# Performance work log

Measured on AMD Instinct MI355X. Metric: run time of the kernel, lower is better.

The kernel has to match this reference:

```python
import jax, jax.numpy as jnp
import numpy as np

N_HEADS = 12
VAL_DIM = 64
TOKEN_DIM = 768


def setup_inputs() -> dict:
    key = jax.random.key(0)
    k1, k2, k3 = jax.random.split(key, 3)
    x = jax.random.normal(k1, (8, 1024, TOKEN_DIM), dtype=jnp.float32)
    W_qkv = jax.random.normal(k2, (TOKEN_DIM, 3 * N_HEADS * VAL_DIM), dtype=jnp.float32) * (TOKEN_DIM ** -0.5)
    W_merge = jax.random.normal(k3, (N_HEADS * VAL_DIM, TOKEN_DIM), dtype=jnp.float32) * ((N_HEADS * VAL_DIM) ** -0.5)
    return {"x": x, "W_qkv": W_qkv, "W_merge": W_merge}


def reference(x, W_qkv, W_merge):
    b, p, _ = x.shape
    scale = VAL_DIM ** -0.5
    qkv = jnp.einsum('bpt,tf->bpf', x, W_qkv)  # (b, p, 3*h*v)
    # einops '(h v k)' -> k is innermost factor
    qkv = qkv.reshape(b, p, N_HEADS, VAL_DIM, 3)
    q = jnp.transpose(qkv[..., 0], (0, 2, 1, 3))  # (b, h, p, v)
    k = jnp.transpose(qkv[..., 1], (0, 2, 1, 3))
    v = jnp.transpose(qkv[..., 2], (0, 2, 1, 3))
    scores = jnp.einsum('bhid,bhjd->bhij', q, k) * scale
    attn = jax.nn.softmax(scores, axis=-1)
    out = jnp.einsum('bhij,bhjd->bhid', attn, v)
    out = jnp.transpose(out, (0, 2, 1, 3)).reshape(b, p, N_HEADS * VAL_DIM)
    return jnp.einsum('bpf,ft->bpt', out, W_merge)
```

## Files before the change

kernel.cpp:

```cpp
#include <hip/hip_runtime.h>
#include <hip/hip_bf16.h>
#include <math.h>


#define B_  8
#define P_  1024
#define T_  768
#define H_  12
#define DV  64
#define F3  2304
#define HD  768
#define PSTR 72

typedef float  f32x4  __attribute__((ext_vector_type(4)));
typedef __bf16 bf16x4 __attribute__((ext_vector_type(4)));
typedef __bf16 bf16x8 __attribute__((ext_vector_type(8)));

#if defined(__has_builtin)
#if __has_builtin(__builtin_amdgcn_exp2f)
#define EX2(x) __builtin_amdgcn_exp2f(x)
#endif
#endif
#ifndef EX2
#define EX2(x) exp2f(x)
#endif

__device__ __forceinline__ void gload16(const void* g, void* l) {
    __builtin_amdgcn_global_load_lds((const __attribute__((address_space(1))) void*)g,
                                     (__attribute__((address_space(3))) void*)l,
                                     16, 0, 0);
}

__global__ __launch_bounds__(256) void k_cvt(const float* __restrict__ src,
                                             __bf16* __restrict__ dst) {
    int bid = blockIdx.x;
    int xcd = bid & 7;
    int seq = bid >> 3;
    int strip = (seq / 12) * 8 + xcd;
    int sub   = seq % 12;
    size_t base = (size_t)strip * (128 * T_) + (size_t)sub * (128 * T_ / 12);
    const float4* s4 = (const float4*)(src + base);
    bf16x4*       d4 = (bf16x4*)(dst + base);
#pragma unroll
    for (int i = 0; i < 8; i++) {
        float4 v = s4[i * 256 + threadIdx.x];
        bf16x4 o = { (__bf16)v.x, (__bf16)v.y, (__bf16)v.z, (__bf16)v.w };
        d4[i * 256 + threadIdx.x] = o;
    }
}

__global__ void k_tcvt(const float* __restrict__ src,
                       __bf16* __restrict__ dst, int R, int C) {
    __shared__ __bf16 tile[32][33];
    int tx = threadIdx.x, ty = threadIdx.y;
    int x = blockIdx.x * 32 + tx;
    int y = blockIdx.y * 32 + ty;
#pragma unroll
    for (int j = 0; j < 32; j += 8)
        tile[ty + j][tx] = (__bf16)src[(size_t)(y + j) * C + x];
    __syncthreads();
    int x2 = blockIdx.y * 32 + tx;
    int y2 = blockIdx.x * 32 + ty;
#pragma unroll
    for (int j = 0; j < 32; j += 8)
        dst[(size_t)(y2 + j) * R + x2] = tile[tx][ty + j];
}

__global__ void k_tcvt_qkv(const float* __restrict__ src,
                           __bf16* __restrict__ dst) {
    __shared__ __bf16 tile[32][33];
    int tx = threadIdx.x, ty = threadIdx.y;
    int n = blockIdx.x * 32 + tx;
    int r = n / 768, idx = n - r * 768;
    int f = (idx >> 6) * 192 + (idx & 63) * 3 + r;
    int t0 = blockIdx.y * 32;
#pragma unroll
    for (int j = 0; j < 32; j += 8)
        tile[ty + j][tx] = (__bf16)src[(size_t)(t0 + ty + j) * F3 + f];
    __syncthreads();
#pragma unroll
    for (int j = 0; j < 32; j += 8)
        dst[(size_t)(blockIdx.x * 32 + ty + j) * T_ + t0 + tx] = tile[tx][ty + j];
}

#define GEMM64_MAINLOOP(Aptr, Btptr, brow, bcol, LD)                             \
    int tid  = threadIdx.x;                                                      \
    int lane = tid & 63, wave = tid >> 6;                                        \
    int l16  = lane & 15, quad = lane >> 4;                                      \
    int wm = (wave >> 1) * 64, wn = (wave & 1) * 64;                             \
    int bro = tid >> 3, bq = tid & 7;                                            \
    f32x4 acc[4][4];                                                             \
    _Pragma("unroll") for (int i = 0; i < 4; i++)                                \
        _Pragma("unroll") for (int j = 0; j < 4; j++)                            \
            acc[i][j] = (f32x4){0.f, 0.f, 0.f, 0.f};                             \
    _Pragma("unroll") for (int it = 0; it < 4; it++) {                           \
        int n = it * 32 + bro;                                                   \
        int gp = bq ^ (n & 7);                                                   \
        gload16((Aptr) + (size_t)((brow) * 128 + n) * (LD) + gp * 8,             \
                LDSb + it * 2048 + tid * 8);                                     \
        gload16((Btptr) + (size_t)((bcol) * 128 + n) * (LD) + gp * 8,            \
                LDSb + 8192 + it * 2048 + tid * 8);                              \
    }                                                                            \
    __syncthreads();                                                             \
    for (int k0 = 0; k0 < (LD); k0 += 64) {                                      \
        int cur = (k0 >> 6) & 1;                                                 \
        __bf16* As = LDSb + cur * 16384;                                         \
        __bf16* Bs = As + 8192;                                                  \
        if (k0 + 64 < (LD)) {                                                    \
            __bf16* Ad = LDSb + (cur ^ 1) * 16384;                               \
            _Pragma("unroll") for (int it = 0; it < 4; it++) {                   \
                int n = it * 32 + bro;                                           \
                int gp = bq ^ (n & 7);                                           \
                gload16((Aptr) + (size_t)((brow) * 128 + n) * (LD) + k0 + 64 + gp * 8, \
                        Ad + it * 2048 + tid * 8);                               \
                gload16((Btptr) + (size_t)((bcol) * 128 + n) * (LD) + k0 + 64 + gp * 8, \
                        Ad + 8192 + it * 2048 + tid * 8);                        \
            }                                                                    \
        }                                                                        \
        _Pragma("unroll") for (int ks = 0; ks < 2; ks++) {                       \
            bf16x8 af[4], bfr[4];                                                \
            _Pragma("unroll") for (int i = 0; i < 4; i++) {                      \
                int r = wm + i * 16 + l16;                                       \
                af[i] = *(const bf16x8*)&As[r * 64 + (((ks * 4 + quad) ^ (r & 7)) << 3)]; \
            }                                                                    \
            _Pragma("unroll") for (int j = 0; j < 4; j++) {                      \
                int r = wn + j * 16 + l16;                                       \
                bfr[j] = *(const bf16x8*)&Bs[r * 64 + (((ks * 4 + quad) ^ (r & 7)) << 3)]; \
            }                                                                    \
            _Pragma("unroll") for (int i = 0; i < 4; i++)                        \
                _Pragma("unroll") for (int j = 0; j < 4; j++)                    \
                    acc[i][j] = __builtin_amdgcn_mfma_f32_16x16x32_bf16(         \
                        af[i], bfr[j], acc[i][j], 0, 0, 0);                      \
        }                                                                        \
        __syncthreads();                                                         \
    }

__global__ __launch_bounds__(256, 2) void k_qkv(const __bf16* __restrict__ Xb,
                                                const __bf16* __restrict__ Wt,
                                                __bf16* __restrict__ Q,
                                                __bf16* __restrict__ K,
                                                __bf16* __restrict__ Vt) {
    __shared__ __align__(16) __bf16 LDSb[2 * 2 * 128 * 64];

    int bid  = blockIdx.x;
    int xcd  = bid & 7;
    int seq  = bid >> 3;
    int brow = (seq / 18) * 8 + xcd;
    int bcol = seq % 18;

    GEMM64_MAINLOOP(Xb, Wt, brow, bcol, T_)

    int region = bcol / 6;
    int b  = brow >> 3;
    int p0 = (brow & 7) * 128;

    if (region < 2) {
        __bf16* D = region == 0 ? Q : K;
        float sc = region == 0 ? 0.1803368801f : 1.0f;
#pragma unroll
        for (int j = 0; j < 4; j++) {
            int idx = (bcol - region * 6) * 128 + wn + j * 16 + l16;
            int h = idx >> 6, v = idx & 63;
            __bf16* Dh = D + ((size_t)(b * H_ + h) * P_) * DV + v;
#pragma unroll
            for (int i = 0; i < 4; i++)
#pragma unroll
                for (int r = 0; r < 4; r++)
                    Dh[(size_t)(p0 + wm + i * 16 + quad * 4 + r) * DV] =
                        (__bf16)(acc[i][j][r] * sc);
        }
    } else {
        __syncthreads();
#pragma unroll
        for (int j = 0; j < 4; j++) {
            int n_loc = wn + j * 16 + l16;
#pragma unroll
            for (int i = 0; i < 4; i++)
#pragma unroll
            for (int r = 0; r < 4; r++) {
                int m_loc = wm + i * 16 + quad * 4 + r;
                int phys  = (m_loc >> 3) ^ (n_loc & 15);
                LDSb[n_loc * 128 + phys * 8 + (m_loc & 7)] = (__bf16)acc[i][j][r];
            }
        }
        __syncthreads();
        int n_loc = tid >> 1, halfm = tid & 1;
        int idx = (bcol - 12) * 128 + n_loc;
        int h = idx >> 6, v = idx & 63;
        __bf16* Dh = Vt + ((size_t)(b * H_ + h) * DV + v) * P_ + p0 + halfm * 64;
#pragma unroll
        for (int i = 0; i < 8; i++) {
            int chunk = halfm * 8 + i;
            int phys  = chunk ^ (n_loc & 15);
            bf16x8 val = *(const bf16x8*)&LDSb[n_loc * 128 + phys * 8];
            *(bf16x8*)(Dh + i * 8) = val;
        }
    }
}

__global__ __launch_bounds__(256, 2) void k_merge(const __bf16* __restrict__ O,
                                                  const __bf16* __restrict__ Wt,
                                                  float* __restrict__ out) {
    __shared__ __align__(16) __bf16 LDSb[2 * 2 * 128 * 64];

    int bid  = blockIdx.x;
    int xcd  = bid & 7;
    int seq  = bid >> 3;
    int brow = (seq / 6) * 8 + xcd;
    int bcol = seq % 6;

    GEMM64_MAINLOOP(O, Wt, brow, bcol, HD)

#pragma unroll
    for (int i = 0; i < 4; i++)
#pragma unroll
        for (int j = 0; j < 4; j++) {
            int col = bcol * 128 + wn + j * 16 + l16;
#pragma unroll
            for (int r = 0; r < 4; r++) {
                size_t row = (size_t)(brow * 128 + wm + i * 16 + quad * 4 + r);
                out[row * HD + col] = acc[i][j][r];
            }
        }
}

__global__ __launch_bounds__(256, 6) void k_attn(const __bf16* __restrict__ Q,
                                                 const __bf16* __restrict__ Kb,
                                                 const __bf16* __restrict__ Vt,
                                                 __bf16* __restrict__ O) {
    __shared__ __align__(16) __bf16 Ks[64 * 64];
    __shared__ __align__(16) __bf16 Vs[64 * 64];
    __shared__ __align__(16) __bf16 Pb[4][16 * PSTR];

    int tid  = threadIdx.x;
    int lane = tid & 63, wave = tid >> 6;
    int l16  = lane & 15, quad = lane >> 4;

    int bid = blockIdx.x;
    int xcd = bid & 7;
    int seq = bid >> 3;
    int bh  = xcd * 12 + (seq % 12);
    int qt  = seq / 12;
    int b   = bh / H_, h = bh % H_;

    const __bf16* Qb  = Q  + (size_t)bh * P_ * DV;
    const __bf16* Kbh = Kb + (size_t)bh * P_ * DV;
    const __bf16* Vbh = Vt + (size_t)bh * DV * P_;
    int m0 = qt * 64 + wave * 16;

    bf16x8 a0 = *(const bf16x8*)(Qb + (size_t)(m0 + l16) * DV + quad * 8);
    bf16x8 a1 = *(const bf16x8*)(Qb + (size_t)(m0 + l16) * DV + 32 + quad * 8);

    int l8 = lane >> 3, q8 = lane & 7;

    bf16x8 ones;
#pragma unroll
    for (int i = 0; i < 8; i++) ones[i] = (__bf16)1.0f;

    __bf16* Pw = &Pb[wave][0];
    f32x4 facc = {0.f, 0.f, 0.f, 0.f};
    f32x4 oacc[4] = {{0.f,0.f,0.f,0.f},{0.f,0.f,0.f,0.f},{0.f,0.f,0.f,0.f},{0.f,0.f,0.f,0.f}};
    int swq = l16 & 7;

    for (int c = 0; c < P_; c += 64) {
        __syncthreads();
#pragma unroll
        for (int i = 0; i < 2; i++) {
            int t = wave * 2 + i;
            int r = t * 8 + l8;
            int j = q8 ^ (r & 7);
            gload16(Kbh + (size_t)(c + r) * DV + j * 8, Ks + t * 512 + lane * 8);
            gload16(Vbh + (size_t)r * P_ + c + j * 8,  Vs + t * 512 + lane * 8);
        }
        __syncthreads();

        f32x4 s[4];
#pragma unroll
        for (int ct = 0; ct < 4; ct++) {
            int R = ct * 16 + l16;
            bf16x8 b0 = *(const bf16x8*)&Ks[R * 64 + ((quad ^ swq) * 8)];
            bf16x8 b1 = *(const bf16x8*)&Ks[R * 64 + (((4 + quad) ^ swq) * 8)];
            f32x4 z = {0.f, 0.f, 0.f, 0.f};
            z = __builtin_amdgcn_mfma_f32_16x16x32_bf16(b0, a0, z, 0, 0, 0);
            s[ct] = __builtin_amdgcn_mfma_f32_16x16x32_bf16(b1, a1, z, 0, 0, 0);
        }

#pragma unroll
        for (int ct = 0; ct < 4; ct++) {
            bf16x4 pk;
#pragma unroll
            for (int r = 0; r < 4; r++)
                pk[r] = (__bf16)EX2(s[ct][r]);
            *(bf16x4*)&Pw[l16 * PSTR + ct * 16 + quad * 4] = pk;
        }

#pragma unroll
        for (int ks = 0; ks < 2; ks++) {
            bf16x8 pfrag = *(const bf16x8*)&Pw[l16 * PSTR + ks * 32 + quad * 8];
            facc = __builtin_amdgcn_mfma_f32_16x16x32_bf16(ones, pfrag, facc, 0, 0, 0);
#pragma unroll
            for (int nt = 0; nt < 4; nt++) {
                int R = nt * 16 + l16;
                bf16x8 av = *(const bf16x8*)&Vs[R * 64 + (((ks * 4 + quad) ^ swq) * 8)];
                oacc[nt] = __builtin_amdgcn_mfma_f32_16x16x32_bf16(av, pfrag, oacc[nt], 0, 0, 0);
            }
        }
    }

    float inv = 1.0f / facc[0];

    int p = m0 + l16;
    __bf16* Orow = O + ((size_t)b * P_ + p) * HD + h * DV;
#pragma unroll
    for (int nt = 0; nt < 4; nt++) {
        bf16x4 o4;
#pragma unroll
        for (int r = 0; r < 4; r++) o4[r] = (__bf16)(oacc[nt][r] * inv);
        *(bf16x4*)&Orow[nt * 16 + quad * 4] = o4;
    }
}

extern "C" void kernel_launch(void* const* d_in, const int* in_sizes, int n_in,
                              void* d_out, int out_size, void* d_ws, size_t ws_size,
                              hipStream_t stream) {
    const float* x      = (const float*)d_in[0];
    const float* wqkv   = (const float*)d_in[1];
    const float* wmerge = (const float*)d_in[2];

    char* w = (char*)d_ws;
    __bf16* Xb  = (__bf16*)w;  w += (size_t)B_ * P_ * T_ * 2;
    __bf16* WqT = (__bf16*)w;  w += (size_t)F3 * T_ * 2;
    __bf16* WmT = (__bf16*)w;  w += (size_t)HD * T_ * 2;
    __bf16* Q   = (__bf16*)w;  w += (size_t)B_ * H_ * P_ * DV * 2;
    __bf16* K   = (__bf16*)w;  w += (size_t)B_ * H_ * P_ * DV * 2;
    __bf16* Vt  = (__bf16*)w;  w += (size_t)B_ * H_ * P_ * DV * 2;
    __bf16* O   = (__bf16*)w;

    hipLaunchKernelGGL(k_cvt, dim3(768), dim3(256), 0, stream, x, Xb);

    dim3 tb(32, 8);
    hipLaunchKernelGGL(k_tcvt_qkv, dim3(F3 / 32, T_ / 32), tb, 0, stream, wqkv, WqT);
    hipLaunchKernelGGL(k_tcvt,     dim3(HD / 32, T_ / 32), tb, 0, stream, wmerge, WmT, T_, HD);

    hipLaunchKernelGGL(k_qkv, dim3((B_ * P_ / 128) * (F3 / 128)), dim3(256), 0, stream,
                       Xb, WqT, Q, K, Vt);

    hipLaunchKernelGGL(k_attn, dim3(B_ * H_ * (P_ / 64)), dim3(256), 0, stream,
                       Q, K, Vt, O);

    hipLaunchKernelGGL(k_merge, dim3((B_ * P_ / 128) * (HD / 128)), dim3(256), 0, stream,
                       O, WmT, (float*)d_out);
}
```

Measured before the change: 183.0 us.

## Double query rows per wave and double-buffer K/V tiles in attention

Each wave in the attention kernel now processes 32 query rows instead of 16, so every K/V tile staged in shared memory feeds twice as many MFMAs, and the grid is halved. K/V tiles are double-buffered: the next 64-key chunk is prefetched into the alternate buffer while the current one is computed, leaving one barrier per iteration instead of two. In exchange, register and LDS use per block rise, occupancy bounds drop from 6 to 3 blocks, and there are fewer blocks to spread across CUs.

```diff
diff --git a/kernel.cpp b/kernel.cpp
--- a/kernel.cpp
+++ b/kernel.cpp
@@ -224,13 +224,12 @@
         }
 }
 
-__global__ __launch_bounds__(256, 6) void k_attn(const __bf16* __restrict__ Q,
+__global__ __launch_bounds__(256, 3) void k_attn(const __bf16* __restrict__ Q,
                                                  const __bf16* __restrict__ Kb,
                                                  const __bf16* __restrict__ Vt,
                                                  __bf16* __restrict__ O) {
-    __shared__ __align__(16) __bf16 Ks[64 * 64];
-    __shared__ __align__(16) __bf16 Vs[64 * 64];
-    __shared__ __align__(16) __bf16 Pb[4][16 * PSTR];
+    __shared__ __align__(16) __bf16 KV[2][8192];
+    __shared__ __align__(16) __bf16 Pb[4][2][16 * PSTR];
 
     int tid  = threadIdx.x;
     int lane = tid & 63, wave = tid >> 6;
@@ -246,10 +245,12 @@
     const __bf16* Qb  = Q  + (size_t)bh * P_ * DV;
     const __bf16* Kbh = Kb + (size_t)bh * P_ * DV;
     const __bf16* Vbh = Vt + (size_t)bh * DV * P_;
-    int m0 = qt * 64 + wave * 16;
-
-    bf16x8 a0 = *(const bf16x8*)(Qb + (size_t)(m0 + l16) * DV + quad * 8);
-    bf16x8 a1 = *(const bf16x8*)(Qb + (size_t)(m0 + l16) * DV + 32 + quad * 8);
+    int m0 = qt * 128 + wave * 32;
+
+    bf16x8 a00 = *(const bf16x8*)(Qb + (size_t)(m0 + l16) * DV + quad * 8);
+    bf16x8 a01 = *(const bf16x8*)(Qb + (size_t)(m0 + l16) * DV + 32 + quad * 8);
+    bf16x8 a10 = *(const bf16x8*)(Qb + (size_t)(m0 + 16 + l16) * DV + quad * 8);
+    bf16x8 a11 = *(const bf16x8*)(Qb + (size_t)(m0 + 16 + l16) * DV + 32 + quad * 8);
 
     int l8 = lane >> 3, q8 = lane & 7;
 
@@ -257,66 +258,110 @@
 #pragma unroll
     for (int i = 0; i < 8; i++) ones[i] = (__bf16)1.0f;
 
-    __bf16* Pw = &Pb[wave][0];
-    f32x4 facc = {0.f, 0.f, 0.f, 0.f};
-    f32x4 oacc[4] = {{0.f,0.f,0.f,0.f},{0.f,0.f,0.f,0.f},{0.f,0.f,0.f,0.f},{0.f,0.f,0.f,0.f}};
+    __bf16* Pw0 = &Pb[wave][0][0];
+    __bf16* Pw1 = &Pb[wave][1][0];
+    f32x4 facc0 = {0.f,0.f,0.f,0.f}, facc1 = {0.f,0.f,0.f,0.f};
+    f32x4 oacc0[4] = {{0.f,0.f,0.f,0.f},{0.f,0.f,0.f,0.f},{0.f,0.f,0.f,0.f},{0.f,0.f,0.f,0.f}};
+    f32x4 oacc1[4] = {{0.f,0.f,0.f,0.f},{0.f,0.f,0.f,0.f},{0.f,0.f,0.f,0.f},{0.f,0.f,0.f,0.f}};
     int swq = l16 & 7;
 
-    for (int c = 0; c < P_; c += 64) {
-        __syncthreads();
-#pragma unroll
-        for (int i = 0; i < 2; i++) {
-            int t = wave * 2 + i;
-            int r = t * 8 + l8;
-            int j = q8 ^ (r & 7);
-            gload16(Kbh + (size_t)(c + r) * DV + j * 8, Ks + t * 512 + lane * 8);
-            gload16(Vbh + (size_t)r * P_ + c + j * 8,  Vs + t * 512 + lane * 8);
-        }
-        __syncthreads();
-
-        f32x4 s[4];
+#pragma unroll
+    for (int i = 0; i < 2; i++) {
+        int t8 = wave * 2 + i;
+        int r  = t8 * 8 + l8;
+        int j  = q8 ^ (r & 7);
+        gload16(Kbh + (size_t)r * DV + j * 8, &KV[0][t8 * 512 + lane * 8]);
+        gload16(Vbh + (size_t)r * P_ + j * 8, &KV[0][4096 + t8 * 512 + lane * 8]);
+    }
+    __syncthreads();
+
+    for (int t = 0; t < 16; t++) {
+        int cur = t & 1;
+        const __bf16* Ks = &KV[cur][0];
+        const __bf16* Vs = &KV[cur][4096];
+
+        if (t < 15) {
+            __bf16* Kd = &KV[cur ^ 1][0];
+            int c = (t + 1) * 64;
+#pragma unroll
+            for (int i = 0; i < 2; i++) {
+                int t8 = wave * 2 + i;
+                int r  = t8 * 8 + l8;
+                int j  = q8 ^ (r & 7);
+                gload16(Kbh + (size_t)(c + r) * DV + j * 8, Kd + t8 * 512 + lane * 8);
+                gload16(Vbh + (size_t)r * P_ + c + j * 8,  Kd + 4096 + t8 * 512 + lane * 8);
+            }
+        }
+
+        f32x4 s0[4], s1[4];
 #pragma unroll
         for (int ct = 0; ct < 4; ct++) {
             int R = ct * 16 + l16;
             bf16x8 b0 = *(const bf16x8*)&Ks[R * 64 + ((quad ^ swq) * 8)];
             bf16x8 b1 = *(const bf16x8*)&Ks[R * 64 + (((4 + quad) ^ swq) * 8)];
-            f32x4 z = {0.f, 0.f, 0.f, 0.f};
-            z = __builtin_amdgcn_mfma_f32_16x16x32_bf16(b0, a0, z, 0, 0, 0);
-            s[ct] = __builtin_amdgcn_mfma_f32_16x16x32_bf16(b1, a1, z, 0, 0, 0);
+            f32x4 z0 = {0.f, 0.f, 0.f, 0.f};
+            z0 = __builtin_amdgcn_mfma_f32_16x16x32_bf16(b0, a00, z0, 0, 0, 0);
+            z0 = __builtin_amdgcn_mfma_f32_16x16x32_bf16(b1, a01, z0, 0, 0, 0);
+            s0[ct] = z0;
+            f32x4 z1 = {0.f, 0.f, 0.f, 0.f};
+            z1 = __builtin_amdgcn_mfma_f32_16x16x32_bf16(b0, a10, z1, 0, 0, 0);
+            z1 = __builtin_amdgcn_mfma_f32_16x16x32_bf16(b1, a11, z1, 0, 0, 0);
+            s1[ct] = z1;
         }
 
 #pragma unroll
         for (int ct = 0; ct < 4; ct++) {
-            bf16x4 pk;
-#pragma unroll
-            for (int r = 0; r < 4; r++)
-                pk[r] = (__bf16)EX2(s[ct][r]);
-            *(bf16x4*)&Pw[l16 * PSTR + ct * 16 + quad * 4] = pk;
+            bf16x4 pk0, pk1;
+#pragma unroll
+            for (int r = 0; r < 4; r++) {
+                pk0[r] = (__bf16)EX2(s0[ct][r]);
+                pk1[r] = (__bf16)EX2(s1[ct][r]);
+            }
+            *(bf16x4*)&Pw0[l16 * PSTR + ct * 16 + quad * 4] = pk0;
+            *(bf16x4*)&Pw1[l16 * PSTR + ct * 16 + quad * 4] = pk1;
         }
 
 #pragma unroll
         for (int ks = 0; ks < 2; ks++) {
-            bf16x8 pfrag = *(const bf16x8*)&Pw[l16 * PSTR + ks * 32 + quad * 8];
-            facc = __builtin_amdgcn_mfma_f32_16x16x32_bf16(ones, pfrag, facc, 0, 0, 0);
+            bf16x8 pf0 = *(const bf16x8*)&Pw0[l16 * PSTR + ks * 32 + quad * 8];
+            bf16x8 pf1 = *(const bf16x8*)&Pw1[l16 * PSTR + ks * 32 + quad * 8];
+            facc0 = __builtin_amdgcn_mfma_f32_16x16x32_bf16(ones, pf0, facc0, 0, 0, 0);
+            facc1 = __builtin_amdgcn_mfma_f32_16x16x32_bf16(ones, pf1, facc1, 0, 0, 0);
 #pragma unroll
             for (int nt = 0; nt < 4; nt++) {
                 int R = nt * 16 + l16;
                 bf16x8 av = *(const bf16x8*)&Vs[R * 64 + (((ks * 4 + quad) ^ swq) * 8)];
-                oacc[nt] = __builtin_amdgcn_mfma_f32_16x16x32_bf16(av, pfrag, oacc[nt], 0, 0, 0);
-            }
-        }
-    }
-
-    float inv = 1.0f / facc[0];
-
-    int p = m0 + l16;
-    __bf16* Orow = O + ((size_t)b * P_ + p) * HD + h * DV;
-#pragma unroll
-    for (int nt = 0; nt < 4; nt++) {
-        bf16x4 o4;
-#pragma unroll
-        for (int r = 0; r < 4; r++) o4[r] = (__bf16)(oacc[nt][r] * inv);
-        *(bf16x4*)&Orow[nt * 16 + quad * 4] = o4;
+                oacc0[nt] = __builtin_amdgcn_mfma_f32_16x16x32_bf16(av, pf0, oacc0[nt], 0, 0, 0);
+                oacc1[nt] = __builtin_amdgcn_mfma_f32_16x16x32_bf16(av, pf1, oacc1[nt], 0, 0, 0);
+            }
+        }
+        __syncthreads();
+    }
+
+    float inv0 = 1.0f / facc0[0];
+    float inv1 = 1.0f / facc1[0];
+
+    {
+        int p = m0 + l16;
+        __bf16* Orow = O + ((size_t)b * P_ + p) * HD + h * DV;
+#pragma unroll
+        for (int nt = 0; nt < 4; nt++) {
+            bf16x4 o4;
+#pragma unroll
+            for (int r = 0; r < 4; r++) o4[r] = (__bf16)(oacc0[nt][r] * inv0);
+            *(bf16x4*)&Orow[nt * 16 + quad * 4] = o4;
+        }
+    }
+    {
+        int p = m0 + 16 + l16;
+        __bf16* Orow = O + ((size_t)b * P_ + p) * HD + h * DV;
+#pragma unroll
+        for (int nt = 0; nt < 4; nt++) {
+            bf16x4 o4;
+#pragma unroll
+            for (int r = 0; r < 4; r++) o4[r] = (__bf16)(oacc1[nt][r] * inv1);
+            *(bf16x4*)&Orow[nt * 16 + quad * 4] = o4;
+        }
     }
 }
 
@@ -345,7 +390,7 @@
     hipLaunchKernelGGL(k_qkv, dim3((B_ * P_ / 128) * (F3 / 128)), dim3(256), 0, stream,
                        Xb, WqT, Q, K, Vt);
 
-    hipLaunchKernelGGL(k_attn, dim3(B_ * H_ * (P_ / 64)), dim3(256), 0, stream,
+    hipLaunchKernelGGL(k_attn, dim3(B_ * H_ * (P_ / 128)), dim3(256), 0, stream,
                        Q, K, Vt, O);
 
     hipLaunchKernelGGL(k_merge, dim3((B_ * P_ / 128) * (HD / 128)), dim3(256), 0, stream,
```

Result: faster. 173.7 us (-5.1%).
